# Kernel optimization log

Measured on AMD Instinct MI355X. Metric: run time of the kernel, lower is better.

## Reference

```python
import jax, jax.numpy as jnp
import numpy as np

N_NODES = 10000
N_EDGES = 320000
D = 256
VOCAB = 28
NEG_SLOPE = 0.2


def _gat_conv(x, ei_src, ei_dst, W, a_src, a_dst, b):
    """PyG GATConv with heads=1, concat=True, self-loops already in ei."""
    h = x @ W                                  # [N, D]
    alpha_s = h @ a_src                        # [N]
    alpha_d = h @ a_dst                        # [N]
    logits = jax.nn.leaky_relu(alpha_s[ei_src] + alpha_d[ei_dst], NEG_SLOPE)  # [E]
    # numerically stable edge softmax per destination node
    m = jax.ops.segment_max(logits, ei_dst, num_segments=N_NODES)
    e = jnp.exp(logits - m[ei_dst])
    denom = jax.ops.segment_sum(e, ei_dst, num_segments=N_NODES)
    alpha = e / denom[ei_dst]                  # [E]
    msgs = alpha[:, None] * h[ei_src]          # [E, D]
    out = jax.ops.segment_sum(msgs, ei_dst, num_segments=N_NODES)
    return out + b


def setup_inputs() -> dict:
    key = jax.random.key(0)
    ks = jax.random.split(key, 16)
    x = jax.random.randint(ks[0], (N_NODES, 1), 0, VOCAB, dtype=jnp.int64)
    edge_index = jax.random.randint(ks[1], (2, N_EDGES), 0, N_NODES, dtype=jnp.int64)
    edge_attr = jax.random.uniform(ks[2], (N_EDGES,), dtype=jnp.float32)
    sc = 1.0 / np.sqrt(D)
    inp = {"x": x, "edge_index": edge_index, "edge_attr": edge_attr,
           "emb": jax.random.normal(ks[3], (VOCAB, D), jnp.float32)}
    for i, k0 in enumerate([4, 7, 10]):
        l = i + 1
        inp[f"W{l}"] = jax.random.normal(ks[k0], (D, D), jnp.float32) * sc
        inp[f"a_src{l}"] = jax.random.normal(ks[k0 + 1], (D,), jnp.float32) * sc
        inp[f"a_dst{l}"] = jax.random.normal(ks[k0 + 2], (D,), jnp.float32) * sc
        inp[f"b{l}"] = jnp.zeros((D,), jnp.float32)
    return inp


def reference(x, edge_index, edge_attr, emb,
              W1, a_src1, a_dst1, b1,
              W2, a_src2, a_dst2, b2,
              W3, a_src3, a_dst3, b3):
    # edge_attr is ignored by GATConv (edge_dim=None), matching PyG behavior.
    # add self loops (PyG default add_self_loops=True)
    loops = jnp.arange(N_NODES, dtype=edge_index.dtype)
    ei_src = jnp.concatenate([edge_index[0], loops])
    ei_dst = jnp.concatenate([edge_index[1], loops])

    h = emb[x.squeeze(-1)]                     # [N, D]
    h = jax.nn.relu(_gat_conv(h, ei_src, ei_dst, W1, a_src1, a_dst1, b1)) + h
    h = jax.nn.relu(_gat_conv(h, ei_src, ei_dst, W2, a_src2, a_dst2, b2)) + h
    out = jax.nn.relu(_gat_conv(h, ei_src, ei_dst, W3, a_src3, a_dst3, b3)) + h
    return out
```

## Files before the change

### kernel.cpp

```cpp
#include <hip/hip_runtime.h>
#include <hip/hip_bf16.h>

#define N_NODES 10000
#define N_EDGES 320000
#define E_TOT (N_EDGES + N_NODES)
#define D 256
#define VOCAB 28
#define NEG 0.2f
#define CAP 96

typedef __attribute__((ext_vector_type(8))) short bf16x8;
typedef __attribute__((ext_vector_type(4))) float f32x4;

__device__ inline float blo(unsigned u) { return __uint_as_float(u << 16); }
__device__ inline float bhi(unsigned u) { return __uint_as_float(u & 0xFFFF0000u); }
__device__ inline unsigned short f2bu(float x) {
  __hip_bfloat16 b = __float2bfloat16(x);
  return *reinterpret_cast<unsigned short*>(&b);
}

__global__ __launch_bounds__(256) void prep_kernel(const float* __restrict__ W0,
                                                   const float* __restrict__ W1,
                                                   const float* __restrict__ W2,
                                                   const float* __restrict__ emb,
                                                   const float* __restrict__ as1,
                                                   const float* __restrict__ ad1,
                                                   const float* __restrict__ as2,
                                                   const float* __restrict__ ad2,
                                                   const float* __restrict__ as3,
                                                   const float* __restrict__ ad3,
                                                   const int* __restrict__ x,
                                                   unsigned short* __restrict__ T1,
                                                   unsigned short* __restrict__ T2,
                                                   unsigned short* __restrict__ hv,
                                                   float4* __restrict__ zbase,
                                                   float* __restrict__ waS2,
                                                   float* __restrict__ waD2,
                                                   float* __restrict__ waS3,
                                                   float* __restrict__ waD3,
                                                   float* __restrict__ al1_s,
                                                   float* __restrict__ al1_d) {
  int tid = threadIdx.x;
  int bid = blockIdx.x;
  if (bid < 32) {
    __shared__ float t[64][65];
    int l = bid >> 4;
    const float* W = (l == 0) ? W1 : W2;
    unsigned short* Wt = (l == 0) ? T1 : T2;
    int sub = bid & 15;
    int bk = (sub & 3) * 64;
    int bn = (sub >> 2) * 64;
    int row = tid >> 2;
    int cq = (tid & 3) * 16;
#pragma unroll
    for (int i = 0; i < 4; ++i) {
      float4 v = *reinterpret_cast<const float4*>(W + (size_t)(bk + row) * D + bn + cq + i * 4);
      t[row][cq + i * 4 + 0] = v.x; t[row][cq + i * 4 + 1] = v.y;
      t[row][cq + i * 4 + 2] = v.z; t[row][cq + i * 4 + 3] = v.w;
    }
    __syncthreads();
#pragma unroll
    for (int i = 0; i < 16; ++i)
      Wt[(size_t)(bn + row) * D + bk + cq + i] = f2bu(t[cq + i][row]);
  } else if (bid < 42) {
    zbase[(bid - 32) * 256 + tid] = float4{0.f, 0.f, 0.f, 0.f};
  } else if (bid == 42 || bid == 43) {
    const float* W = (bid == 42) ? W1 : W2;
    const float* as = (bid == 42) ? as2 : as3;
    const float* ad = (bid == 42) ? ad2 : ad3;
    float* oS = (bid == 42) ? waS2 : waS3;
    float* oD = (bid == 42) ? waD2 : waD3;
    float s = 0.f, d = 0.f;
    const float* row = W + (size_t)tid * D;
    for (int n = 0; n < D; ++n) {
      float w = row[n];
      s += w * as[n];
      d += w * ad[n];
    }
    oS[tid] = s; oD[tid] = d;
  } else if (bid == 44) {
    __shared__ float ws1[256], wd1[256], avs[VOCAB], avd[VOCAB];
    {
      float s = 0.f, d = 0.f;
      const float* row = W0 + (size_t)tid * D;
      for (int n = 0; n < D; ++n) {
        float w = row[n];
        s += w * as1[n];
        d += w * ad1[n];
      }
      ws1[tid] = s; wd1[tid] = d;
    }
    __syncthreads();
    int wid = tid >> 6, lane = tid & 63;
    for (int t = wid; t < VOCAB; t += 4) {
      float ps = 0.f, pd = 0.f;
      for (int k = lane; k < D; k += 64) {
        float e = emb[(size_t)t * D + k];
        ps += e * ws1[k];
        pd += e * wd1[k];
      }
#pragma unroll
      for (int off = 32; off; off >>= 1) {
        ps += __shfl_xor(ps, off);
        pd += __shfl_xor(pd, off);
      }
      if (lane == 0) { avs[t] = ps; avd[t] = pd; }
    }
    __syncthreads();
    for (int n = tid; n < N_NODES; n += 256) {
      int t = x[n];
      al1_s[n] = avs[t];
      al1_d[n] = avd[t];
    }
  } else {
    int tok = bid - 45;
    float s = 0.f;
    for (int k = 0; k < D; ++k)
      s += emb[(size_t)tok * D + k] * W0[(size_t)k * D + tid];
    hv[(size_t)tok * D + tid] = f2bu(s);
  }
}

__global__ __launch_bounds__(256) void scatter_kernel(const int* __restrict__ ei,
                                                      int* __restrict__ counts,
                                                      int* __restrict__ csr) {
  int e = blockIdx.x * 256 + threadIdx.x;
  if (e >= E_TOT) return;
  int src, dst;
  if (e < N_EDGES) { src = ei[e]; dst = ei[N_EDGES + e]; }
  else             { src = e - N_EDGES; dst = src; }
  int pos = atomicAdd(&counts[dst], 1);
  csr[dst * CAP + pos] = src;
}

__global__ __launch_bounds__(256) void gemm_kernel(const unsigned short* __restrict__ Asrc,
                                                   const unsigned short* __restrict__ Bt,
                                                   unsigned short* __restrict__ C) {
  __shared__ unsigned short As[64][72];
  __shared__ unsigned short Bs[64][72];
  int t = threadIdx.x;
  int bm = blockIdx.x * 64;
  int bn = blockIdx.y * 64;
  int lane = t & 63, wid = t >> 6;
  int wr = (wid >> 1) * 32, wc = (wid & 1) * 32;
  int fr = lane & 15, fk = (lane >> 4) * 8;

  f32x4 acc[2][2] = {};
  for (int k0 = 0; k0 < D; k0 += 64) {
#pragma unroll
    for (int c = t; c < 512; c += 256) {
      int row = c >> 3, cc = (c & 7) * 8;
      int gr = bm + row;
      uint4 v = {0u, 0u, 0u, 0u};
      if (gr < N_NODES)
        v = *reinterpret_cast<const uint4*>(Asrc + (size_t)gr * D + k0 + cc);
      *reinterpret_cast<uint4*>(&As[row][cc]) = v;
      uint4 w = *reinterpret_cast<const uint4*>(Bt + (size_t)(bn + row) * D + k0 + cc);
      *reinterpret_cast<uint4*>(&Bs[row][cc]) = w;
    }
    __syncthreads();
#pragma unroll
    for (int ks = 0; ks < 2; ++ks) {
      bf16x8 a0 = *reinterpret_cast<const bf16x8*>(&As[wr + fr][ks * 32 + fk]);
      bf16x8 a1 = *reinterpret_cast<const bf16x8*>(&As[wr + 16 + fr][ks * 32 + fk]);
      bf16x8 b0 = *reinterpret_cast<const bf16x8*>(&Bs[wc + fr][ks * 32 + fk]);
      bf16x8 b1 = *reinterpret_cast<const bf16x8*>(&Bs[wc + 16 + fr][ks * 32 + fk]);
      acc[0][0] = __builtin_amdgcn_mfma_f32_16x16x32_bf16(a0, b0, acc[0][0], 0, 0, 0);
      acc[0][1] = __builtin_amdgcn_mfma_f32_16x16x32_bf16(a0, b1, acc[0][1], 0, 0, 0);
      acc[1][0] = __builtin_amdgcn_mfma_f32_16x16x32_bf16(a1, b0, acc[1][0], 0, 0, 0);
      acc[1][1] = __builtin_amdgcn_mfma_f32_16x16x32_bf16(a1, b1, acc[1][1], 0, 0, 0);
    }
    __syncthreads();
  }

  int orow = (lane >> 4) * 4;
#pragma unroll
  for (int m = 0; m < 2; ++m)
#pragma unroll
    for (int n = 0; n < 2; ++n)
#pragma unroll
      for (int r = 0; r < 4; ++r) {
        int gr = bm + wr + m * 16 + orow + r;
        if (gr < N_NODES)
          C[(size_t)gr * D + bn + wc + n * 16 + fr] = f2bu(acc[m][n][r]);
      }
}

#define EDGE2(J)                                                                       \
  {                                                                                    \
    int s_ = ssh[wid][(J) + half];                                                     \
    float w_ = wsh[wid][(J) + half];                                                   \
    uint4 q_ = *reinterpret_cast<const uint4*>(hb_base + (size_t)s_ * D);              \
    a0 += w_ * blo(q_.x); a1 += w_ * bhi(q_.x); a2 += w_ * blo(q_.y);                  \
    a3 += w_ * bhi(q_.y); a4 += w_ * blo(q_.z); a5 += w_ * bhi(q_.z);                  \
    a6 += w_ * blo(q_.w); a7 += w_ * bhi(q_.w);                                        \
  }

__global__ __launch_bounds__(256, 4) void agg_kernel(const int* __restrict__ csr,
                                                     const int* __restrict__ counts,
                                                     const float* __restrict__ al_s,
                                                     const float* __restrict__ al_d,
                                                     const unsigned short* __restrict__ hlin,
                                                     const float* __restrict__ bias,
                                                     const float* __restrict__ h_prev,
                                                     const int* __restrict__ xv,
                                                     const float* __restrict__ emb,
                                                     float* __restrict__ out_f,
                                                     unsigned short* __restrict__ out_b,
                                                     const float* __restrict__ waS_n,
                                                     const float* __restrict__ waD_n,
                                                     float* __restrict__ aln_s,
                                                     float* __restrict__ aln_d,
                                                     const int* __restrict__ idx_tab) {
  __shared__ int   ssh[4][CAP];
  __shared__ float wsh[4][CAP];
  int wid = threadIdx.x >> 6, lane = threadIdx.x & 63;
  int dst = blockIdx.x * 4 + wid;
  if (dst >= N_NODES) return;
  int cnt = counts[dst];
  const int* rowp = csr + (size_t)dst * CAP;
  float ad = al_d[dst];

  float m = -1e30f;
  for (int j = lane; j < cnt; j += 64) {
    int s = rowp[j];
    ssh[wid][j] = idx_tab ? idx_tab[s] : s;
    float v = al_s[s] + ad;
    v = (v >= 0.f) ? v : NEG * v;
    wsh[wid][j] = v;
    m = fmaxf(m, v);
  }
#pragma unroll
  for (int off = 32; off; off >>= 1) m = fmaxf(m, __shfl_xor(m, off));

  float denom = 0.f;
  for (int j = lane; j < cnt; j += 64) {
    float w = __expf(wsh[wid][j] - m);
    wsh[wid][j] = w;
    denom += w;
  }
#pragma unroll
  for (int off = 32; off; off >>= 1) denom += __shfl_xor(denom, off);
  float inv = 1.0f / denom;

  int half = lane >> 5, fl = lane & 31;
  const unsigned short* hb_base = hlin + fl * 8;
  float a0 = 0.f, a1 = 0.f, a2 = 0.f, a3 = 0.f;
  float a4 = 0.f, a5 = 0.f, a6 = 0.f, a7 = 0.f;
  int j = 0;
  for (; j + 16 <= cnt; j += 16) {
    EDGE2(j + 0) EDGE2(j + 2) EDGE2(j + 4) EDGE2(j + 6)
    EDGE2(j + 8) EDGE2(j + 10) EDGE2(j + 12) EDGE2(j + 14)
  }
  for (; j + 8 <= cnt; j += 8) {
    EDGE2(j + 0) EDGE2(j + 2) EDGE2(j + 4) EDGE2(j + 6)
  }
  for (; j < cnt; j += 2) {
    int jj = j + half;
    bool valid = jj < cnt;
    int s0 = ssh[wid][valid ? jj : 0];
    float w0 = valid ? wsh[wid][jj] : 0.f;
    uint4 q0 = *reinterpret_cast<const uint4*>(hb_base + (size_t)s0 * D);
    a0 += w0 * blo(q0.x); a1 += w0 * bhi(q0.x); a2 += w0 * blo(q0.y); a3 += w0 * bhi(q0.y);
    a4 += w0 * blo(q0.z); a5 += w0 * bhi(q0.z); a6 += w0 * blo(q0.w); a7 += w0 * bhi(q0.w);
  }
  a0 += __shfl_xor(a0, 32); a1 += __shfl_xor(a1, 32);
  a2 += __shfl_xor(a2, 32); a3 += __shfl_xor(a3, 32);
  a4 += __shfl_xor(a4, 32); a5 += __shfl_xor(a5, 32);
  a6 += __shfl_xor(a6, 32); a7 += __shfl_xor(a7, 32);
  float b0 = half ? a4 : a0, b1 = half ? a5 : a1;
  float b2 = half ? a6 : a2, b3 = half ? a7 : a3;
  int fb = fl * 8 + half * 4;
  const float* hp_row = h_prev ? (h_prev + (size_t)dst * D)
                               : (emb + (size_t)xv[dst] * D);
  float4 bb = *reinterpret_cast<const float4*>(bias + fb);
  float4 hp = *reinterpret_cast<const float4*>(hp_row + fb);
  float o0 = fmaxf(b0 * inv + bb.x, 0.f) + hp.x;
  float o1 = fmaxf(b1 * inv + bb.y, 0.f) + hp.y;
  float o2 = fmaxf(b2 * inv + bb.z, 0.f) + hp.z;
  float o3 = fmaxf(b3 * inv + bb.w, 0.f) + hp.w;
  float4 o = {o0, o1, o2, o3};
  *reinterpret_cast<float4*>(out_f + (size_t)dst * D + fb) = o;
  if (out_b) {
    uint2 p;
    p.x = (unsigned)f2bu(o0) | ((unsigned)f2bu(o1) << 16);
    p.y = (unsigned)f2bu(o2) | ((unsigned)f2bu(o3) << 16);
    *reinterpret_cast<uint2*>(out_b + (size_t)dst * D + fb) = p;
  }
  if (waS_n) {
    float4 s4 = *reinterpret_cast<const float4*>(waS_n + fb);
    float4 d4 = *reinterpret_cast<const float4*>(waD_n + fb);
    float ps = o0 * s4.x + o1 * s4.y + o2 * s4.z + o3 * s4.w;
    float pd = o0 * d4.x + o1 * d4.y + o2 * d4.z + o3 * d4.w;
#pragma unroll
    for (int off = 32; off; off >>= 1) {
      ps += __shfl_xor(ps, off);
      pd += __shfl_xor(pd, off);
    }
    if (lane == 0) { aln_s[dst] = ps; aln_d[dst] = pd; }
  }
}

extern "C" void kernel_launch(void* const* d_in, const int* in_sizes, int n_in,
                              void* d_out, int out_size, void* d_ws, size_t ws_size,
                              hipStream_t stream) {
  const int*   x   = (const int*)d_in[0];
  const int*   ei  = (const int*)d_in[1];
  const float* emb = (const float*)d_in[3];
  const float* W[3]    = {(const float*)d_in[4],  (const float*)d_in[8],  (const float*)d_in[12]};
  const float* asrc[3] = {(const float*)d_in[5],  (const float*)d_in[9],  (const float*)d_in[13]};
  const float* adst[3] = {(const float*)d_in[6],  (const float*)d_in[10], (const float*)d_in[14]};
  const float* bias[3] = {(const float*)d_in[7],  (const float*)d_in[11], (const float*)d_in[15]};

  char* ws = (char*)d_ws;
  float*          h    = (float*)(ws);
  unsigned short* hb   = (unsigned short*)(ws + 10240000);
  unsigned short* hlin = (unsigned short*)(ws + 15360000);
  unsigned short* Wt1  = (unsigned short*)(ws + 20480000);
  unsigned short* Wt2  = (unsigned short*)(ws + 20611072);
  float* al_s[3] = {(float*)(ws + 20873216), (float*)(ws + 20914176), (float*)(ws + 20955136)};
  float* al_d[3] = {(float*)(ws + 20996096), (float*)(ws + 21037056), (float*)(ws + 21078016)};
  int* counts = (int*)(ws + 21118976);
  int* csr    = (int*)(ws + 21241856);
  unsigned short* hv = (unsigned short*)(ws + 25081856);
  float* waS2 = (float*)(ws + 25096192);
  float* waD2 = (float*)(ws + 25097216);
  float* waS3 = (float*)(ws + 25098240);
  float* waD3 = (float*)(ws + 25099264);

  prep_kernel<<<73, 256, 0, stream>>>(W[0], W[1], W[2], emb,
                                      asrc[0], adst[0], asrc[1], adst[1], asrc[2], adst[2],
                                      x, Wt1, Wt2, hv,
                                      (float4*)counts, waS2, waD2, waS3, waD3,
                                      al_s[0], al_d[0]);

  scatter_kernel<<<(E_TOT + 255) / 256, 256, 0, stream>>>(ei, counts, csr);

  agg_kernel<<<2500, 256, 0, stream>>>(csr, counts, al_s[0], al_d[0],
                                       hv, bias[0], nullptr, x, emb,
                                       h, hb, waS2, waD2, al_s[1], al_d[1], x);

  dim3 gemm_grid(157, 4);
  gemm_kernel<<<gemm_grid, 256, 0, stream>>>(hb, Wt1, hlin);
  agg_kernel<<<2500, 256, 0, stream>>>(csr, counts, al_s[1], al_d[1],
                                       hlin, bias[1], h, nullptr, nullptr,
                                       h, hb, waS3, waD3, al_s[2], al_d[2], nullptr);
  gemm_kernel<<<gemm_grid, 256, 0, stream>>>(hb, Wt2, hlin);
  agg_kernel<<<2500, 256, 0, stream>>>(csr, counts, al_s[2], al_d[2],
                                       hlin, bias[2], h, nullptr, nullptr,
                                       (float*)d_out, nullptr, nullptr, nullptr,
                                       nullptr, nullptr, nullptr);
}
```

Before: 126.1 us.

## Split each destination node's edge aggregation across two wavefronts

The aggregation kernel now assigns two wavefronts per destination node instead of one. Each wave handles half the edge list, and the partial max, denominator and feature accumulators are combined through shared memory with block barriers. The grid doubles to 5000 blocks and the unroll depth drops from 16 to 8. The aim is more memory-level parallelism and shorter per-wave latency chains for the gather-bound loop, at the cost of three __syncthreads, extra shared-memory traffic, and removal of the min-occupancy launch bound.

Result: slower. 128.9 us (+2.2%).

```diff
diff --git a/kernel.cpp b/kernel.cpp
--- a/kernel.cpp
+++ b/kernel.cpp
@@ -188,116 +188,138 @@
 
 #define EDGE2(J)                                                                       \
   {                                                                                    \
-    int s_ = ssh[wid][(J) + half];                                                     \
-    float w_ = wsh[wid][(J) + half];                                                   \
+    int s_ = ssh[ds][(J) + half];                                                      \
+    float w_ = wsh[ds][(J) + half];                                                    \
     uint4 q_ = *reinterpret_cast<const uint4*>(hb_base + (size_t)s_ * D);              \
     a0 += w_ * blo(q_.x); a1 += w_ * bhi(q_.x); a2 += w_ * blo(q_.y);                  \
     a3 += w_ * bhi(q_.y); a4 += w_ * blo(q_.z); a5 += w_ * bhi(q_.z);                  \
     a6 += w_ * blo(q_.w); a7 += w_ * bhi(q_.w);                                        \
   }
 
-__global__ __launch_bounds__(256, 4) void agg_kernel(const int* __restrict__ csr,
-                                                     const int* __restrict__ counts,
-                                                     const float* __restrict__ al_s,
-                                                     const float* __restrict__ al_d,
-                                                     const unsigned short* __restrict__ hlin,
-                                                     const float* __restrict__ bias,
-                                                     const float* __restrict__ h_prev,
-                                                     const int* __restrict__ xv,
-                                                     const float* __restrict__ emb,
-                                                     float* __restrict__ out_f,
-                                                     unsigned short* __restrict__ out_b,
-                                                     const float* __restrict__ waS_n,
-                                                     const float* __restrict__ waD_n,
-                                                     float* __restrict__ aln_s,
-                                                     float* __restrict__ aln_d,
-                                                     const int* __restrict__ idx_tab) {
-  __shared__ int   ssh[4][CAP];
-  __shared__ float wsh[4][CAP];
+__global__ __launch_bounds__(256) void agg_kernel(const int* __restrict__ csr,
+                                                  const int* __restrict__ counts,
+                                                  const float* __restrict__ al_s,
+                                                  const float* __restrict__ al_d,
+                                                  const unsigned short* __restrict__ hlin,
+                                                  const float* __restrict__ bias,
+                                                  const float* __restrict__ h_prev,
+                                                  const int* __restrict__ xv,
+                                                  const float* __restrict__ emb,
+                                                  float* __restrict__ out_f,
+                                                  unsigned short* __restrict__ out_b,
+                                                  const float* __restrict__ waS_n,
+                                                  const float* __restrict__ waD_n,
+                                                  float* __restrict__ aln_s,
+                                                  float* __restrict__ aln_d,
+                                                  const int* __restrict__ idx_tab) {
+  __shared__ int   ssh[2][CAP];
+  __shared__ float wsh[2][CAP];
+  __shared__ float redm[2][2];
+  __shared__ float redd[2][2];
+  __shared__ float accsh[2][8][64];
   int wid = threadIdx.x >> 6, lane = threadIdx.x & 63;
-  int dst = blockIdx.x * 4 + wid;
-  if (dst >= N_NODES) return;
+  int ds = wid >> 1;
+  int sub = wid & 1;
+  int dst = blockIdx.x * 2 + ds;
   int cnt = counts[dst];
+  int cnt2 = (cnt + 1) >> 1;
+  int beg = sub * cnt2;
+  int end = sub ? cnt : cnt2;
   const int* rowp = csr + (size_t)dst * CAP;
   float ad = al_d[dst];
 
   float m = -1e30f;
-  for (int j = lane; j < cnt; j += 64) {
+  for (int j = beg + lane; j < end; j += 64) {
     int s = rowp[j];
-    ssh[wid][j] = idx_tab ? idx_tab[s] : s;
+    ssh[ds][j] = idx_tab ? idx_tab[s] : s;
     float v = al_s[s] + ad;
     v = (v >= 0.f) ? v : NEG * v;
-    wsh[wid][j] = v;
+    wsh[ds][j] = v;
     m = fmaxf(m, v);
   }
 #pragma unroll
   for (int off = 32; off; off >>= 1) m = fmaxf(m, __shfl_xor(m, off));
+  if (lane == 0) redm[ds][sub] = m;
+  __syncthreads();
+  m = fmaxf(redm[ds][0], redm[ds][1]);
 
   float denom = 0.f;
-  for (int j = lane; j < cnt; j += 64) {
-    float w = __expf(wsh[wid][j] - m);
-    wsh[wid][j] = w;
+  for (int j = beg + lane; j < end; j += 64) {
+    float w = __expf(wsh[ds][j] - m);
+    wsh[ds][j] = w;
     denom += w;
   }
 #pragma unroll
   for (int off = 32; off; off >>= 1) denom += __shfl_xor(denom, off);
-  float inv = 1.0f / denom;
+  if (lane == 0) redd[ds][sub] = denom;
+  __syncthreads();
+  float inv = 1.0f / (redd[ds][0] + redd[ds][1]);
 
   int half = lane >> 5, fl = lane & 31;
   const unsigned short* hb_base = hlin + fl * 8;
   float a0 = 0.f, a1 = 0.f, a2 = 0.f, a3 = 0.f;
   float a4 = 0.f, a5 = 0.f, a6 = 0.f, a7 = 0.f;
-  int j = 0;
-  for (; j + 16 <= cnt; j += 16) {
+  int j = beg;
+  for (; j + 8 <= end; j += 8) {
     EDGE2(j + 0) EDGE2(j + 2) EDGE2(j + 4) EDGE2(j + 6)
-    EDGE2(j + 8) EDGE2(j + 10) EDGE2(j + 12) EDGE2(j + 14)
-  }
-  for (; j + 8 <= cnt; j += 8) {
-    EDGE2(j + 0) EDGE2(j + 2) EDGE2(j + 4) EDGE2(j + 6)
-  }
-  for (; j < cnt; j += 2) {
+  }
+  for (; j < end; j += 2) {
     int jj = j + half;
-    bool valid = jj < cnt;
-    int s0 = ssh[wid][valid ? jj : 0];
-    float w0 = valid ? wsh[wid][jj] : 0.f;
+    bool valid = jj < end;
+    int s0 = ssh[ds][valid ? jj : beg];
+    float w0 = valid ? wsh[ds][jj] : 0.f;
     uint4 q0 = *reinterpret_cast<const uint4*>(hb_base + (size_t)s0 * D);
     a0 += w0 * blo(q0.x); a1 += w0 * bhi(q0.x); a2 += w0 * blo(q0.y); a3 += w0 * bhi(q0.y);
     a4 += w0 * blo(q0.z); a5 += w0 * bhi(q0.z); a6 += w0 * blo(q0.w); a7 += w0 * bhi(q0.w);
   }
-  a0 += __shfl_xor(a0, 32); a1 += __shfl_xor(a1, 32);
-  a2 += __shfl_xor(a2, 32); a3 += __shfl_xor(a3, 32);
-  a4 += __shfl_xor(a4, 32); a5 += __shfl_xor(a5, 32);
-  a6 += __shfl_xor(a6, 32); a7 += __shfl_xor(a7, 32);
-  float b0 = half ? a4 : a0, b1 = half ? a5 : a1;
-  float b2 = half ? a6 : a2, b3 = half ? a7 : a3;
-  int fb = fl * 8 + half * 4;
-  const float* hp_row = h_prev ? (h_prev + (size_t)dst * D)
-                               : (emb + (size_t)xv[dst] * D);
-  float4 bb = *reinterpret_cast<const float4*>(bias + fb);
-  float4 hp = *reinterpret_cast<const float4*>(hp_row + fb);
-  float o0 = fmaxf(b0 * inv + bb.x, 0.f) + hp.x;
-  float o1 = fmaxf(b1 * inv + bb.y, 0.f) + hp.y;
-  float o2 = fmaxf(b2 * inv + bb.z, 0.f) + hp.z;
-  float o3 = fmaxf(b3 * inv + bb.w, 0.f) + hp.w;
-  float4 o = {o0, o1, o2, o3};
-  *reinterpret_cast<float4*>(out_f + (size_t)dst * D + fb) = o;
-  if (out_b) {
-    uint2 p;
-    p.x = (unsigned)f2bu(o0) | ((unsigned)f2bu(o1) << 16);
-    p.y = (unsigned)f2bu(o2) | ((unsigned)f2bu(o3) << 16);
-    *reinterpret_cast<uint2*>(out_b + (size_t)dst * D + fb) = p;
-  }
-  if (waS_n) {
-    float4 s4 = *reinterpret_cast<const float4*>(waS_n + fb);
-    float4 d4 = *reinterpret_cast<const float4*>(waD_n + fb);
-    float ps = o0 * s4.x + o1 * s4.y + o2 * s4.z + o3 * s4.w;
-    float pd = o0 * d4.x + o1 * d4.y + o2 * d4.z + o3 * d4.w;
-#pragma unroll
-    for (int off = 32; off; off >>= 1) {
-      ps += __shfl_xor(ps, off);
-      pd += __shfl_xor(pd, off);
-    }
-    if (lane == 0) { aln_s[dst] = ps; aln_d[dst] = pd; }
+
+  if (sub == 1) {
+    accsh[ds][0][lane] = a0; accsh[ds][1][lane] = a1;
+    accsh[ds][2][lane] = a2; accsh[ds][3][lane] = a3;
+    accsh[ds][4][lane] = a4; accsh[ds][5][lane] = a5;
+    accsh[ds][6][lane] = a6; accsh[ds][7][lane] = a7;
+  }
+  __syncthreads();
+  if (sub == 0) {
+    a0 += accsh[ds][0][lane]; a1 += accsh[ds][1][lane];
+    a2 += accsh[ds][2][lane]; a3 += accsh[ds][3][lane];
+    a4 += accsh[ds][4][lane]; a5 += accsh[ds][5][lane];
+    a6 += accsh[ds][6][lane]; a7 += accsh[ds][7][lane];
+    a0 += __shfl_xor(a0, 32); a1 += __shfl_xor(a1, 32);
+    a2 += __shfl_xor(a2, 32); a3 += __shfl_xor(a3, 32);
+    a4 += __shfl_xor(a4, 32); a5 += __shfl_xor(a5, 32);
+    a6 += __shfl_xor(a6, 32); a7 += __shfl_xor(a7, 32);
+    float b0 = half ? a4 : a0, b1 = half ? a5 : a1;
+    float b2 = half ? a6 : a2, b3 = half ? a7 : a3;
+    int fb = fl * 8 + half * 4;
+    const float* hp_row = h_prev ? (h_prev + (size_t)dst * D)
+                                 : (emb + (size_t)xv[dst] * D);
+    float4 bb = *reinterpret_cast<const float4*>(bias + fb);
+    float4 hp = *reinterpret_cast<const float4*>(hp_row + fb);
+    float o0 = fmaxf(b0 * inv + bb.x, 0.f) + hp.x;
+    float o1 = fmaxf(b1 * inv + bb.y, 0.f) + hp.y;
+    float o2 = fmaxf(b2 * inv + bb.z, 0.f) + hp.z;
+    float o3 = fmaxf(b3 * inv + bb.w, 0.f) + hp.w;
+    float4 o = {o0, o1, o2, o3};
+    *reinterpret_cast<float4*>(out_f + (size_t)dst * D + fb) = o;
+    if (out_b) {
+      uint2 p;
+      p.x = (unsigned)f2bu(o0) | ((unsigned)f2bu(o1) << 16);
+      p.y = (unsigned)f2bu(o2) | ((unsigned)f2bu(o3) << 16);
+      *reinterpret_cast<uint2*>(out_b + (size_t)dst * D + fb) = p;
+    }
+    if (waS_n) {
+      float4 s4 = *reinterpret_cast<const float4*>(waS_n + fb);
+      float4 d4 = *reinterpret_cast<const float4*>(waD_n + fb);
+      float ps = o0 * s4.x + o1 * s4.y + o2 * s4.z + o3 * s4.w;
+      float pd = o0 * d4.x + o1 * d4.y + o2 * d4.z + o3 * d4.w;
+#pragma unroll
+      for (int off = 32; off; off >>= 1) {
+        ps += __shfl_xor(ps, off);
+        pd += __shfl_xor(pd, off);
+      }
+      if (lane == 0) { aln_s[dst] = ps; aln_d[dst] = pd; }
+    }
   }
 }
 
@@ -336,17 +358,17 @@
 
   scatter_kernel<<<(E_TOT + 255) / 256, 256, 0, stream>>>(ei, counts, csr);
 
-  agg_kernel<<<2500, 256, 0, stream>>>(csr, counts, al_s[0], al_d[0],
+  agg_kernel<<<5000, 256, 0, stream>>>(csr, counts, al_s[0], al_d[0],
                                        hv, bias[0], nullptr, x, emb,
                                        h, hb, waS2, waD2, al_s[1], al_d[1], x);
 
   dim3 gemm_grid(157, 4);
   gemm_kernel<<<gemm_grid, 256, 0, stream>>>(hb, Wt1, hlin);
-  agg_kernel<<<2500, 256, 0, stream>>>(csr, counts, al_s[1], al_d[1],
+  agg_kernel<<<5000, 256, 0, stream>>>(csr, counts, al_s[1], al_d[1],
                                        hlin, bias[1], h, nullptr, nullptr,
                                        h, hb, waS3, waD3, al_s[2], al_d[2], nullptr);
   gemm_kernel<<<gemm_grid, 256, 0, stream>>>(hb, Wt2, hlin);
-  agg_kernel<<<2500, 256, 0, stream>>>(csr, counts, al_s[2], al_d[2],
+  agg_kernel<<<5000, 256, 0, stream>>>(csr, counts, al_s[2], al_d[2],
                                        hlin, bias[2], h, nullptr, nullptr,
                                        (float*)d_out, nullptr, nullptr, nullptr,
                                        nullptr, nullptr, nullptr);
```
